# Kernel optimization log

Hardware: AMD Instinct MI355X
Metric: run time of the kernel (lower is better)

## Reference

```python
import jax, jax.numpy as jnp
import numpy as np
from jax import lax
jax.config.update("jax_enable_x64", True)

B, N, H = 64, 2048, 64
FS, FC, C = 1.0e10, 3.0e11, 3.0e8
N_LAYERS, CG_STEPS = 4, 5
F32 = jnp.float32
_T64 = jnp.arange(N, dtype=jnp.float64) / FS  # time grid, float64 (FIX 7)


def _gru_dir(xproj, whh, bhh, reverse):
    # xproj: [B,N,3H] = x @ Wih^T + bih precomputed; torch gate order (r,z,n)
    def step(h, xp):
        gh = h @ whh.T + bhh
        r = jax.nn.sigmoid(xp[:, :H] + gh[:, :H])
        z = jax.nn.sigmoid(xp[:, H:2 * H] + gh[:, H:2 * H])
        n = jnp.tanh(xp[:, 2 * H:] + r * gh[:, 2 * H:])
        h2 = (1.0 - z) * n + z * h
        return h2, h2
    xs = jnp.swapaxes(xproj, 0, 1)
    if reverse:
        xs = xs[::-1]
    h0 = jnp.zeros((xproj.shape[0], H), xproj.dtype)
    _, hs = lax.scan(step, h0, xs)
    if reverse:
        hs = hs[::-1]
    return jnp.swapaxes(hs, 0, 1)


def _channel_diag(theta, bussgang_gain):
    # float64 phase: tau = R/c (single trip), phase = 2*pi*fc*(tau + (v/c)t + 0.5(a/c)t^2)
    th = theta.astype(jnp.float64)
    tau = th[:, 0:1] / C
    td = th[:, 1:2] / C
    tdd = th[:, 2:3] / C
    t = _T64[None, :]
    phase = 2.0 * np.pi * FC * (tau + td * t + 0.5 * tdd * t ** 2)
    h = jnp.exp(-1j * phase).astype(jnp.complex64)
    return h * bussgang_gain


def _forward(y_real, y_imag, theta, meta_features, gamma_eff, scale_slope, bussgang_gain,
             reg_w1, reg_b1, reg_w2, reg_b2, pw1, pb1, ln_g, ln_b, pw2, pb2, pw3, pb3,
             gru_wih_f, gru_whh_f, gru_bih_f, gru_bhh_f, gru_wih_b, gru_whh_b, gru_bih_b, gru_bhh_b,
             hw1, hb1, hw2, hb2, phase_bias):
    y_q = lax.complex(y_real, y_imag)
    # PhysicsEncoder.get_approx_fim_info
    reg = jax.nn.softplus(jax.nn.relu(gamma_eff @ reg_w1.T + reg_b1) @ reg_w2.T + reg_b2) + 1e-6  # [B,1]
    log_vol = -jnp.log(reg) * 3.0
    # PilotNavigator
    h1 = meta_features @ pw1.T + pb1
    mu = jnp.mean(h1, -1, keepdims=True)
    var = jnp.var(h1, -1, keepdims=True)
    h1 = (h1 - mu) / jnp.sqrt(var + 1e-5) * ln_g + ln_b
    h2 = jax.nn.relu(jax.nn.relu(h1) @ pw2.T + pb2)
    logits = h2 @ pw3.T + pb3
    g_PN = jax.nn.sigmoid(logits[:, 0:1])
    g_NL = jax.nn.softplus(logits[:, 1:2]) + 0.5
    physics_brake = jax.nn.sigmoid((log_vol - (-15.0)) * 5.0)
    g_grad = jax.nn.sigmoid(logits[:, 2:3]) * physics_brake
    # diagonal channel
    h_eff = _channel_diag(theta, bussgang_gain)  # [B,N] c64
    hh = (jnp.conj(h_eff) * h_eff).real  # |h|^2, [B,N]
    lam = reg  # damping from reg_net
    feats_raw = jnp.stack([y_q.real, y_q.imag], -1)  # [B,N,2]
    bias = lax.complex(jnp.cos(phase_bias), -jnp.sin(phase_bias))  # exp(-j*phase_bias)
    x_est = jnp.zeros((B, N), jnp.complex64)
    for _ in range(N_LAYERS):  # shared weights across layers
        # RiemannianPNTracker
        reliable = jnp.mean(jnp.abs(x_est)) > 0.1
        x_norm = x_est / (jnp.abs(x_est) + 1e-6)
        resid = y_q * jnp.conj(x_norm)
        feats = jnp.where(reliable, jnp.stack([resid.real, resid.imag], -1), feats_raw)
        xp_f = feats @ gru_wih_f.T + gru_bih_f
        xp_b = feats @ gru_wih_b.T + gru_bih_b
        rnn_out = jnp.concatenate([_gru_dir(xp_f, gru_whh_f, gru_bhh_f, False),
                                   _gru_dir(xp_b, gru_whh_b, gru_bhh_b, True)], axis=-1)  # [B,N,2H]
        cs = jax.nn.relu(rnn_out @ hw1.T + hb1) @ hw2.T + hb2  # [B,N,2]
        cos_p, sin_p = cs[..., 0], cs[..., 1]
        mag = jnp.sqrt(cos_p ** 2 + sin_p ** 2 + 1e-8)
        derot = lax.complex(cos_p / mag, -sin_p / mag) * bias
        eff = (1.0 - g_PN) + g_PN * derot
        eff = eff / (jnp.abs(eff) + 1e-8)
        z_in = y_q * eff
        # BussgangRefiner
        beta = scale_slope * g_NL  # [B,1]
        zr = jnp.tanh(beta * z_in.real)
        zi = jnp.tanh(beta * z_in.imag)
        z_out = lax.complex(zr, zi)
        onsager = jnp.mean(beta * (1 - zr ** 2) + beta * (1 - zi ** 2), axis=1, keepdims=True) * 0.5
        z_corr = z_out - onsager * x_est  # AMP-style Onsager correction
        # Unrolled CG: (H^H H + lam I) x = H^H z_corr, warm start x_est
        b = jnp.conj(h_eff) * z_corr
        diagA = hh + lam  # [B,N] real
        x = x_est
        r = b - diagA * x
        p = r
        rs = jnp.sum(jnp.conj(r) * r, axis=1, keepdims=True).real
        for _ in range(CG_STEPS):
            Ap = diagA * p
            alpha = rs / (jnp.sum(jnp.conj(p) * Ap, axis=1, keepdims=True).real + 1e-20)
            x = x + alpha * p
            r = r - alpha * Ap
            rs_new = jnp.sum(jnp.conj(r) * r, axis=1, keepdims=True).real
            p = r + (rs_new / (rs + 1e-20)) * p
            rs = rs_new
        x_est = (1.0 - g_grad) * x_est + g_grad * x
    return jnp.stack([x_est.real, x_est.imag], axis=-1).astype(F32)  # [B,N,2]


def setup_inputs() -> dict:
    key = jax.random.key(0)
    ks = jax.random.split(key, 20)
    def rn(k, shape, s=0.1):
        return jax.random.normal(k, shape, dtype=F32) * s
    u = jax.random.uniform(ks[0], (B, 3), dtype=F32)
    theta = jnp.stack([1e4 + u[:, 0] * 9e4, (u[:, 1] - 0.5) * 200.0, (u[:, 2] - 0.5) * 20.0], axis=1)
    return {
        "y_real": jax.random.normal(ks[1], (B, N), dtype=F32),
        "y_imag": jax.random.normal(ks[2], (B, N), dtype=F32),
        "theta": theta,
        "meta_features": jax.random.normal(ks[3], (B, 6), dtype=F32),
        "gamma_eff": jax.random.uniform(ks[4], (B, 1), dtype=F32),
        "scale_slope": jnp.asarray(1.0, F32),
        "bussgang_gain": jnp.asarray(1.0, F32),
        "reg_w1": rn(ks[5], (16, 1)), "reg_b1": jnp.zeros((16,), F32),
        "reg_w2": rn(ks[6], (1, 16)), "reg_b2": jnp.zeros((1,), F32),
        "pw1": rn(ks[7], (64, 6)), "pb1": jnp.zeros((64,), F32),
        "ln_g": jnp.ones((64,), F32), "ln_b": jnp.zeros((64,), F32),
        "pw2": rn(ks[8], (32, 64)), "pb2": jnp.zeros((32,), F32),
        "pw3": rn(ks[9], (4, 32)), "pb3": jnp.zeros((4,), F32),
        "gru_wih_f": rn(ks[10], (3 * H, 2)), "gru_whh_f": rn(ks[11], (3 * H, H)),
        "gru_bih_f": jnp.zeros((3 * H,), F32), "gru_bhh_f": jnp.zeros((3 * H,), F32),
        "gru_wih_b": rn(ks[12], (3 * H, 2)), "gru_whh_b": rn(ks[13], (3 * H, H)),
        "gru_bih_b": jnp.zeros((3 * H,), F32), "gru_bhh_b": jnp.zeros((3 * H,), F32),
        "hw1": rn(ks[14], (H // 2, 2 * H)), "hb1": jnp.zeros((H // 2,), F32),
        "hw2": rn(ks[15], (2, H // 2)), "hb2": jnp.zeros((2,), F32),
        "phase_bias": jnp.asarray(-1.5708, F32),
    }


def reference(y_real, y_imag, theta, meta_features, gamma_eff, scale_slope, bussgang_gain,
              reg_w1, reg_b1, reg_w2, reg_b2, pw1, pb1, ln_g, ln_b, pw2, pb2, pw3, pb3,
              gru_wih_f, gru_whh_f, gru_bih_f, gru_bhh_f, gru_wih_b, gru_whh_b, gru_bih_b, gru_bhh_b,
              hw1, hb1, hw2, hb2, phase_bias):
    return _forward(y_real, y_imag, theta, meta_features, gamma_eff, scale_slope, bussgang_gain,
                    reg_w1, reg_b1, reg_w2, reg_b2, pw1, pb1, ln_g, ln_b, pw2, pb2, pw3, pb3,
                    gru_wih_f, gru_whh_f, gru_bih_f, gru_bhh_f, gru_wih_b, gru_whh_b, gru_bih_b, gru_bhh_b,
                    hw1, hb1, hw2, hb2, phase_bias)
```

## Files before the change

kernel.cpp:

```cpp
#include <hip/hip_runtime.h>
#include <hip/hip_bf16.h>
#include <math.h>

#define BB 64
#define NN 2048
#define HID 64
#define NLAYERS 4
#define CGS 5

#define WS_X      0
#define WS_FEATS  (2*BB*NN)
#define WS_CS     (4*BB*NN)
#define WS_HEFF   (6*BB*NN)
#define WS_HH     (8*BB*NN)
#define WS_LAM    (9*BB*NN)
#define WS_GPN    (9*BB*NN + BB)
#define WS_GNL    (9*BB*NN + 2*BB)
#define WS_GGR    (9*BB*NN + 3*BB)
#define WS_REL    (9*BB*NN + 4*BB)
#define WS_RNN    (9*BB*NN + 4*BB + 64)

typedef float v2f __attribute__((ext_vector_type(2)));

__device__ __forceinline__ float sigf(float x) { return 1.0f / (1.0f + expf(-x)); }
__device__ __forceinline__ float softplusf(float x) {
    return fmaxf(x, 0.0f) + log1pf(expf(-fabsf(x)));
}
__device__ __forceinline__ float fsig(float x) {
    return __builtin_amdgcn_rcpf(1.0f + __expf(-x));
}
__device__ __forceinline__ float ftanh(float x) {
    float ax = fabsf(x);
    float e = __expf(-2.0f * ax);
    float t = (1.0f - e) * __builtin_amdgcn_rcpf(1.0f + e);
    return copysignf(t, x);
}

__global__ __launch_bounds__(64) void k_scalars(
    const float* __restrict__ gamma, const float* __restrict__ meta,
    const float* __restrict__ rw1, const float* __restrict__ rb1,
    const float* __restrict__ rw2, const float* __restrict__ rb2,
    const float* __restrict__ pw1, const float* __restrict__ pb1,
    const float* __restrict__ lng, const float* __restrict__ lnb,
    const float* __restrict__ pw2, const float* __restrict__ pb2,
    const float* __restrict__ pw3, const float* __restrict__ pb3,
    float* __restrict__ ws)
{
    int b = threadIdx.x;
    if (b < NLAYERS) ws[WS_REL + b] = 0.0f;
    if (b >= BB) return;

    float g = gamma[b];
    float acc = rb2[0];
    for (int j = 0; j < 16; j++) {
        float t = fmaxf(fmaf(g, rw1[j], rb1[j]), 0.0f);
        acc = fmaf(t, rw2[j], acc);
    }
    float lam = softplusf(acc) + 1e-6f;
    float log_vol = -logf(lam) * 3.0f;

    float m[6];
    for (int i = 0; i < 6; i++) m[i] = meta[b * 6 + i];
    float h1[64];
    float mu = 0.0f;
    for (int j = 0; j < 64; j++) {
        float a = pb1[j];
        for (int i = 0; i < 6; i++) a = fmaf(m[i], pw1[j * 6 + i], a);
        h1[j] = a; mu += a;
    }
    mu *= (1.0f / 64.0f);
    float var = 0.0f;
    for (int j = 0; j < 64; j++) { float d = h1[j] - mu; var = fmaf(d, d, var); }
    var *= (1.0f / 64.0f);
    float inv = 1.0f / sqrtf(var + 1e-5f);
    for (int j = 0; j < 64; j++) h1[j] = (h1[j] - mu) * inv * lng[j] + lnb[j];

    float h2[32];
    for (int k = 0; k < 32; k++) {
        float a = pb2[k];
        for (int j = 0; j < 64; j++) {
            float r = fmaxf(h1[j], 0.0f);
            a = fmaf(r, pw2[k * 64 + j], a);
        }
        h2[k] = fmaxf(a, 0.0f);
    }
    float lg[3];
    for (int o = 0; o < 3; o++) {
        float a = pb3[o];
        for (int k = 0; k < 32; k++) a = fmaf(h2[k], pw3[o * 32 + k], a);
        lg[o] = a;
    }
    float gPN = sigf(lg[0]);
    float gNL = softplusf(lg[1]) + 0.5f;
    float brake = sigf((log_vol + 15.0f) * 5.0f);
    float ggr = sigf(lg[2]) * brake;

    ws[WS_LAM + b] = lam;
    ws[WS_GPN + b] = gPN;
    ws[WS_GNL + b] = gNL;
    ws[WS_GGR + b] = ggr;
}

__global__ __launch_bounds__(256) void k_chan(
    const float* __restrict__ theta, const float* __restrict__ bg,
    float* __restrict__ ws)
{
    int idx = blockIdx.x * 256 + threadIdx.x;
    int b = idx >> 11;
    int n = idx & (NN - 1);
    double th0 = (double)theta[b * 3 + 0];
    double th1 = (double)theta[b * 3 + 1];
    double th2 = (double)theta[b * 3 + 2];
    const double Cc = 300000000.0, FS = 10000000000.0, FC = 300000000000.0;
    double tau = th0 / Cc, td = th1 / Cc, tdd = th2 / Cc;
    double t = (double)n / FS;
    double phase = 6.283185307179586 * FC * (tau + td * t + 0.5 * tdd * t * t);
    double s, c;
    sincos(phase, &s, &c);
    float gain = bg[0];
    float hr = (float)c * gain;
    float hi = (float)(-s) * gain;
    ws[WS_HEFF + 2 * idx] = hr;
    ws[WS_HEFF + 2 * idx + 1] = hi;
    ws[WS_HH + idx] = hr * hr + hi * hi;
    ws[WS_X + 2 * idx] = 0.0f;
    ws[WS_X + 2 * idx + 1] = 0.0f;
}

__global__ __launch_bounds__(256) void k_feats(
    const float* __restrict__ yr, const float* __restrict__ yi,
    float* __restrict__ ws, int layer)
{
    float rel = ws[WS_REL + layer] * (1.0f / (BB * NN));
    bool reliable = rel > 0.1f;
    int idx = blockIdx.x * 256 + threadIdx.x;
    float Yr = yr[idx], Yi = yi[idx];
    float fr, fi;
    if (reliable) {
        float xr = ws[WS_X + 2 * idx], xi = ws[WS_X + 2 * idx + 1];
        float a = sqrtf(xr * xr + xi * xi) + 1e-6f;
        float nr = xr / a, ni = xi / a;
        fr = Yr * nr + Yi * ni;
        fi = Yi * nr - Yr * ni;
    } else {
        fr = Yr; fi = Yi;
    }
    ws[WS_FEATS + 2 * idx] = fr;
    ws[WS_FEATS + 2 * idx + 1] = fi;
}

__global__ __attribute__((amdgpu_flat_work_group_size(192, 192), amdgpu_waves_per_eu(1, 1)))
void k_gru(
    const float* __restrict__ feats,
    const float* __restrict__ wih_f, const float* __restrict__ whh_f,
    const float* __restrict__ bih_f, const float* __restrict__ bhh_f,
    const float* __restrict__ wih_b, const float* __restrict__ whh_b,
    const float* __restrict__ bih_b, const float* __restrict__ bhh_b,
    float* __restrict__ rnn)
{
    __shared__ float sf[2 * NN];
    __shared__ __align__(16) float sh[HID];
    __shared__ float srz[2][HID];

    int chain = blockIdx.x;
    int b = chain >> 1;
    int d = chain & 1;
    int tid = threadIdx.x;
    int lane = tid & 63;
    int w = tid >> 6;

    const float* wih = d ? wih_b : wih_f;
    const float* whh = d ? whh_b : whh_f;
    const float* bih = d ? bih_b : bih_f;
    const float* bhh = d ? bhh_b : bhh_f;

    int row = w * 64 + lane;
    v2f W[32];
    {
        const float4* wp = reinterpret_cast<const float4*>(whh + (size_t)row * 64);
        #pragma unroll
        for (int q = 0; q < 16; q++) {
            float4 v = wp[q];
            W[2 * q]     = (v2f){v.x, v.y};
            W[2 * q + 1] = (v2f){v.z, v.w};
        }
    }
    float wi0 = wih[row * 2], wi1 = wih[row * 2 + 1];
    float bi = bih[row];
    float bh = bhh[row];

    {
        const float4* fp = reinterpret_cast<const float4*>(feats + (size_t)b * 2 * NN);
        float4* sp = reinterpret_cast<float4*>(sf);
        for (int j = tid; j < NN / 2; j += 192) sp[j] = fp[j];
    }
    float h = 0.0f;
    if (w == 2) sh[lane] = 0.0f;
    __syncthreads();

    const float2* fptr = reinterpret_cast<const float2*>(sf) + (d ? (NN - 1) : 0);
    int fstep = d ? -1 : 1;
    float* optr = rnn + (size_t)b * NN * 128 + (size_t)(d ? (NN - 1) : 0) * 128
                + d * 64 + lane;
    ptrdiff_t ostep = d ? -128 : 128;

    #pragma unroll 2
    for (int s = 0; s < NN; s++) {
        float2 f = *fptr;
        fptr += fstep;
        float xp = fmaf(f.y, wi1, fmaf(f.x, wi0, bi));

        v2f a0 = {0, 0}, a1 = {0, 0};
        #pragma unroll
        for (int q = 0; q < 16; q++) {
            float4 hv = *reinterpret_cast<const float4*>(&sh[4 * q]);
            a0 = __builtin_elementwise_fma(W[2 * q],     (v2f){hv.x, hv.y}, a0);
            a1 = __builtin_elementwise_fma(W[2 * q + 1], (v2f){hv.z, hv.w}, a1);
        }
        v2f as = a0 + a1;
        float gh = bh + (as.x + as.y);

        if (w < 2) srz[w][lane] = fsig(xp + gh);

        asm volatile("s_waitcnt lgkmcnt(0)" ::: "memory");
        __builtin_amdgcn_s_barrier();
        asm volatile("" ::: "memory");

        if (w == 2) {
            float r = srz[0][lane], z = srz[1][lane];
            float n = ftanh(fmaf(r, gh, xp));
            h = (1.0f - z) * n + z * h;
            sh[lane] = h;
            *optr = h;
        }
        optr += ostep;

        asm volatile("s_waitcnt lgkmcnt(0)" ::: "memory");
        __builtin_amdgcn_s_barrier();
        asm volatile("" ::: "memory");
    }
}

__global__ __launch_bounds__(256) void k_head(
    const float* __restrict__ rnn,
    const float* __restrict__ hw1, const float* __restrict__ hb1,
    const float* __restrict__ hw2, const float* __restrict__ hb2,
    float* __restrict__ cs)
{
    __shared__ float sw1[32 * 128];
    __shared__ float sb1[32], sw2[64], sb2[2];
    int tid = threadIdx.x;
    for (int i = tid; i < 4096; i += 256) sw1[i] = hw1[i];
    if (tid < 32) sb1[tid] = hb1[tid];
    if (tid < 64) sw2[tid] = hw2[tid];
    if (tid < 2)  sb2[tid] = hb2[tid];
    __syncthreads();

    int idx = blockIdx.x * 256 + tid;
    float x[128];
    const float4* rp = reinterpret_cast<const float4*>(rnn + (size_t)idx * 128);
    #pragma unroll
    for (int q = 0; q < 32; q++) {
        float4 v = rp[q];
        x[q * 4 + 0] = v.x;
        x[q * 4 + 1] = v.y;
        x[q * 4 + 2] = v.z;
        x[q * 4 + 3] = v.w;
    }

    float c0 = sb2[0], c1 = sb2[1];
    for (int k = 0; k < 32; k++) {
        float a = sb1[k];
        #pragma unroll
        for (int j = 0; j < 128; j++) a = fmaf(x[j], sw1[k * 128 + j], a);
        a = fmaxf(a, 0.0f);
        c0 = fmaf(a, sw2[k], c0);
        c1 = fmaf(a, sw2[32 + k], c1);
    }
    cs[2 * idx] = c0;
    cs[2 * idx + 1] = c1;
}

__device__ __forceinline__ float block_sum(float v, float* sred, int tid) {
    #pragma unroll
    for (int o = 32; o > 0; o >>= 1) v += __shfl_down(v, o, 64);
    __syncthreads();
    if ((tid & 63) == 0) sred[tid >> 6] = v;
    __syncthreads();
    return sred[0] + sred[1] + sred[2] + sred[3];
}

__global__ __launch_bounds__(256) void k_solve(
    const float* __restrict__ yr, const float* __restrict__ yi,
    float* __restrict__ ws,
    const float* __restrict__ scale_slope, const float* __restrict__ phase_bias,
    float* __restrict__ out, int layer)
{
    __shared__ float sred[4];
    int b = blockIdx.x, tid = threadIdx.x;
    float lam = ws[WS_LAM + b], gPN = ws[WS_GPN + b];
    float gNL = ws[WS_GNL + b], gg = ws[WS_GGR + b];
    float beta = scale_slope[0] * gNL;
    float pb = phase_bias[0];
    float bsr = cosf(pb), bsi = -sinf(pb);

    float Yr[8], Yi[8], Hr[8], Hi[8], dA[8], Xr[8], Xi[8], Br[8], Bi[8];
    float ons = 0.0f;
    #pragma unroll
    for (int i = 0; i < 8; i++) {
        int idx = b * NN + tid + i * 256;
        float yr_ = yr[idx], yi_ = yi[idx];
        float c = ws[WS_CS + 2 * idx], s = ws[WS_CS + 2 * idx + 1];
        float mag = sqrtf(c * c + s * s + 1e-8f);
        float dr = c / mag, di = -s / mag;
        float der = dr * bsr - di * bsi;
        float dei = dr * bsi + di * bsr;
        float er = 1.0f - gPN + gPN * der;
        float ei = gPN * dei;
        float ea = sqrtf(er * er + ei * ei) + 1e-8f;
        er /= ea; ei /= ea;
        float zri = yr_ * er - yi_ * ei;
        float zii = yr_ * ei + yi_ * er;
        float zr = tanhf(beta * zri);
        float zi = tanhf(beta * zii);
        ons += beta * (1.0f - zr * zr) + beta * (1.0f - zi * zi);
        Yr[i] = yr_; Yi[i] = yi_;
        Hr[i] = ws[WS_HEFF + 2 * idx]; Hi[i] = ws[WS_HEFF + 2 * idx + 1];
        dA[i] = ws[WS_HH + idx] + lam;
        Xr[i] = ws[WS_X + 2 * idx]; Xi[i] = ws[WS_X + 2 * idx + 1];
        Br[i] = zr; Bi[i] = zi;
    }
    float onsager = block_sum(ons, sred, tid) * (0.5f / NN);

    #pragma unroll
    for (int i = 0; i < 8; i++) {
        float zcr = Br[i] - onsager * Xr[i];
        float zci = Bi[i] - onsager * Xi[i];
        Br[i] = Hr[i] * zcr + Hi[i] * zci;
        Bi[i] = Hr[i] * zci - Hi[i] * zcr;
    }

    float xr[8], xi[8], Rr[8], Ri[8], Pr[8], Pi[8];
    float rs_p = 0.0f;
    #pragma unroll
    for (int i = 0; i < 8; i++) {
        xr[i] = Xr[i]; xi[i] = Xi[i];
        Rr[i] = Br[i] - dA[i] * xr[i];
        Ri[i] = Bi[i] - dA[i] * xi[i];
        Pr[i] = Rr[i]; Pi[i] = Ri[i];
        rs_p += Rr[i] * Rr[i] + Ri[i] * Ri[i];
    }
    float rs = block_sum(rs_p, sred, tid);

    for (int it = 0; it < CGS; it++) {
        float pap = 0.0f;
        #pragma unroll
        for (int i = 0; i < 8; i++) pap += dA[i] * (Pr[i] * Pr[i] + Pi[i] * Pi[i]);
        float alpha = rs / (block_sum(pap, sred, tid) + 1e-20f);
        float rsn_p = 0.0f;
        #pragma unroll
        for (int i = 0; i < 8; i++) {
            xr[i] += alpha * Pr[i]; xi[i] += alpha * Pi[i];
            Rr[i] -= alpha * dA[i] * Pr[i];
            Ri[i] -= alpha * dA[i] * Pi[i];
            rsn_p += Rr[i] * Rr[i] + Ri[i] * Ri[i];
        }
        float rsn = block_sum(rsn_p, sred, tid);
        float bsc = rsn / (rs + 1e-20f);
        #pragma unroll
        for (int i = 0; i < 8; i++) {
            Pr[i] = Rr[i] + bsc * Pr[i];
            Pi[i] = Ri[i] + bsc * Pi[i];
        }
        rs = rsn;
    }

    float relp = 0.0f;
    float* dstx = (layer == NLAYERS - 1) ? out : (ws + WS_X);
    #pragma unroll
    for (int i = 0; i < 8; i++) {
        int idx = b * NN + tid + i * 256;
        float nr = (1.0f - gg) * Xr[i] + gg * xr[i];
        float ni = (1.0f - gg) * Xi[i] + gg * xi[i];
        dstx[2 * idx] = nr;
        dstx[2 * idx + 1] = ni;
        if (layer < NLAYERS - 1) {
            ws[WS_X + 2 * idx] = nr;
            ws[WS_X + 2 * idx + 1] = ni;
        }
        relp += sqrtf(nr * nr + ni * ni);
    }
    float relsum = block_sum(relp, sred, tid);
    if (tid == 0 && layer + 1 < NLAYERS) atomicAdd(ws + WS_REL + layer + 1, relsum);
}

extern "C" void kernel_launch(void* const* d_in, const int* in_sizes, int n_in,
                              void* d_out, int out_size, void* d_ws, size_t ws_size,
                              hipStream_t stream)
{
    const float* yr    = (const float*)d_in[0];
    const float* yi    = (const float*)d_in[1];
    const float* theta = (const float*)d_in[2];
    const float* meta  = (const float*)d_in[3];
    const float* gamma = (const float*)d_in[4];
    const float* sslope= (const float*)d_in[5];
    const float* bgain = (const float*)d_in[6];
    const float* rw1   = (const float*)d_in[7];
    const float* rb1   = (const float*)d_in[8];
    const float* rw2   = (const float*)d_in[9];
    const float* rb2   = (const float*)d_in[10];
    const float* pw1   = (const float*)d_in[11];
    const float* pb1   = (const float*)d_in[12];
    const float* lng   = (const float*)d_in[13];
    const float* lnb   = (const float*)d_in[14];
    const float* pw2   = (const float*)d_in[15];
    const float* pb2   = (const float*)d_in[16];
    const float* pw3   = (const float*)d_in[17];
    const float* pb3   = (const float*)d_in[18];
    const float* wih_f = (const float*)d_in[19];
    const float* whh_f = (const float*)d_in[20];
    const float* bih_f = (const float*)d_in[21];
    const float* bhh_f = (const float*)d_in[22];
    const float* wih_b = (const float*)d_in[23];
    const float* whh_b = (const float*)d_in[24];
    const float* bih_b = (const float*)d_in[25];
    const float* bhh_b = (const float*)d_in[26];
    const float* hw1   = (const float*)d_in[27];
    const float* hb1   = (const float*)d_in[28];
    const float* hw2   = (const float*)d_in[29];
    const float* hb2   = (const float*)d_in[30];
    const float* pbias = (const float*)d_in[31];

    float* ws = (float*)d_ws;
    float* out = (float*)d_out;
    float* rnn = ws + WS_RNN;

    k_scalars<<<1, 64, 0, stream>>>(gamma, meta, rw1, rb1, rw2, rb2,
                                    pw1, pb1, lng, lnb, pw2, pb2, pw3, pb3, ws);
    k_chan<<<(BB * NN) / 256, 256, 0, stream>>>(theta, bgain, ws);

    for (int L = 0; L < NLAYERS; L++) {
        k_feats<<<(BB * NN) / 256, 256, 0, stream>>>(yr, yi, ws, L);
        k_gru<<<BB * 2, 192, 0, stream>>>(ws + WS_FEATS,
                                          wih_f, whh_f, bih_f, bhh_f,
                                          wih_b, whh_b, bih_b, bhh_b, rnn);
        k_head<<<(BB * NN) / 256, 256, 0, stream>>>(rnn, hw1, hb1, hw2, hb2,
                                                    ws + WS_CS);
        k_solve<<<BB, 256, 0, stream>>>(yr, yi, ws, sslope, pbias, out, L);
    }
}
```

Measured before the change: 3.376 ms.

## Replicate GRU gate math across waves to drop one barrier per step

Each of the three waves now computes the full gate update redundantly, using its own per-wave copy of h and all three input projections. This removes the second block barrier per timestep and the serialised r/z handoff into the third wave. Gate pre-activations are double-buffered in shared memory so one barrier per step is enough to keep the waves consistent. The cost is three times the transcendental work per step and extra LDS traffic, in exchange for a shorter serial critical path in the 2048-step recurrence.

New measurement: 3.701 ms. +9.6%, slower.

```diff
diff --git a/kernel.cpp b/kernel.cpp
--- a/kernel.cpp
+++ b/kernel.cpp
@@ -159,8 +159,8 @@
     float* __restrict__ rnn)
 {
     __shared__ float sf[2 * NN];
-    __shared__ __align__(16) float sh[HID];
-    __shared__ float srz[2][HID];
+    __shared__ __align__(16) float hb[3][HID];
+    __shared__ float P[2][3][HID];
 
     int chain = blockIdx.x;
     int b = chain >> 1;
@@ -185,8 +185,10 @@
             W[2 * q + 1] = (v2f){v.z, v.w};
         }
     }
-    float wi0 = wih[row * 2], wi1 = wih[row * 2 + 1];
-    float bi = bih[row];
+    float wir0 = wih[lane * 2],            wir1 = wih[lane * 2 + 1];
+    float wiz0 = wih[(64 + lane) * 2],     wiz1 = wih[(64 + lane) * 2 + 1];
+    float win0 = wih[(128 + lane) * 2],    win1 = wih[(128 + lane) * 2 + 1];
+    float bir = bih[lane], biz = bih[64 + lane], bin = bih[128 + lane];
     float bh = bhh[row];
 
     {
@@ -195,7 +197,6 @@
         for (int j = tid; j < NN / 2; j += 192) sp[j] = fp[j];
     }
     float h = 0.0f;
-    if (w == 2) sh[lane] = 0.0f;
     __syncthreads();
 
     const float2* fptr = reinterpret_cast<const float2*>(sf) + (d ? (NN - 1) : 0);
@@ -206,38 +207,42 @@
 
     #pragma unroll 2
     for (int s = 0; s < NN; s++) {
+        int pb = s & 1;
+
+        hb[w][lane] = h;
         float2 f = *fptr;
         fptr += fstep;
-        float xp = fmaf(f.y, wi1, fmaf(f.x, wi0, bi));
+        asm volatile("s_waitcnt lgkmcnt(0)" ::: "memory");
+
+        float xpr = fmaf(f.y, wir1, fmaf(f.x, wir0, bir));
+        float xpz = fmaf(f.y, wiz1, fmaf(f.x, wiz0, biz));
+        float xpn = fmaf(f.y, win1, fmaf(f.x, win0, bin));
 
         v2f a0 = {0, 0}, a1 = {0, 0};
         #pragma unroll
         for (int q = 0; q < 16; q++) {
-            float4 hv = *reinterpret_cast<const float4*>(&sh[4 * q]);
+            float4 hv = *reinterpret_cast<const float4*>(&hb[w][4 * q]);
             a0 = __builtin_elementwise_fma(W[2 * q],     (v2f){hv.x, hv.y}, a0);
             a1 = __builtin_elementwise_fma(W[2 * q + 1], (v2f){hv.z, hv.w}, a1);
         }
         v2f as = a0 + a1;
-        float gh = bh + (as.x + as.y);
-
-        if (w < 2) srz[w][lane] = fsig(xp + gh);
+        P[pb][w][lane] = bh + (as.x + as.y);
 
         asm volatile("s_waitcnt lgkmcnt(0)" ::: "memory");
         __builtin_amdgcn_s_barrier();
         asm volatile("" ::: "memory");
 
-        if (w == 2) {
-            float r = srz[0][lane], z = srz[1][lane];
-            float n = ftanh(fmaf(r, gh, xp));
-            h = (1.0f - z) * n + z * h;
-            sh[lane] = h;
-            *optr = h;
-        }
+        float GHr = P[pb][0][lane];
+        float GHz = P[pb][1][lane];
+        float GHn = P[pb][2][lane];
+
+        float r = fsig(xpr + GHr);
+        float z = fsig(xpz + GHz);
+        float n = ftanh(fmaf(r, GHn, xpn));
+        h = (1.0f - z) * n + z * h;
+
+        if (w == 2) *optr = h;
         optr += ostep;
-
-        asm volatile("s_waitcnt lgkmcnt(0)" ::: "memory");
-        __builtin_amdgcn_s_barrier();
-        asm volatile("" ::: "memory");
     }
 }
 
```
